# Performance work log

Hardware: AMD Instinct MI355X
Metric: run time of the kernel (lower is better)

## Reference

```python
import jax, jax.numpy as jnp
import numpy as np
import itertools

GRID_NUM = 12
VOXEL_SIZE = 0.12
OFFSET = GRID_NUM * VOXEL_SIZE / 2.0  # 0.72
G3 = GRID_NUM ** 3


def setup_inputs() -> dict:
    key = jax.random.key(0)
    k0, k1, k2, k3 = jax.random.split(key, 4)
    B, L0, L1, C = 4, 2048, 1024, 64
    x0 = jax.random.normal(k0, (B, L0, C), dtype=jnp.float32)
    x1 = jax.random.normal(k1, (B, L1, C), dtype=jnp.float32)
    # positions in [-0.3, 0.3) so delta_pos + OFFSET lies inside the grid [0, 1.44)
    pos0 = (jax.random.uniform(k2, (B, L0, 3), dtype=jnp.float32) - 0.5) * 0.6
    pos1 = (jax.random.uniform(k3, (B, L1, 3), dtype=jnp.float32) - 0.5) * 0.6
    return {"x0": x0, "x1": x1, "pos0": pos0, "pos1": pos1}


def _p2g_trilinear(pos, prob, seg, num_seg):
    """Trilinear point-to-grid splat.
    pos: (N,3) continuous coords in grid units' metric space; prob: (N,); seg: (N,) int segment id.
    Returns (num_seg, G3)."""
    c = pos / VOXEL_SIZE - 0.5          # voxel-center coordinates
    base = jnp.floor(c)
    frac = c - base                      # (N,3) in [0,1)
    base = base.astype(jnp.int32)
    out = jnp.zeros((num_seg * G3,), dtype=prob.dtype)
    for corner in itertools.product((0, 1), repeat=3):
        idx = base + jnp.asarray(corner, dtype=jnp.int32)  # (N,3)
        w = prob
        for d in range(3):
            w = w * (frac[:, d] if corner[d] else (1.0 - frac[:, d]))
        valid = jnp.all((idx >= 0) & (idx < GRID_NUM), axis=-1)
        flat = seg * G3 + idx[:, 0] * (GRID_NUM * GRID_NUM) + idx[:, 1] * GRID_NUM + idx[:, 2]
        flat = jnp.where(valid, flat, 0)
        out = out.at[flat].add(jnp.where(valid, w, 0.0))
    return out.reshape(num_seg, G3)


def reference(x0, x1, pos0, pos1):
    B, L0, C = x0.shape
    L1 = x1.shape[1]
    # scaled correlation + row softmax (stable; max-subtraction is math-identical)
    corr = jnp.einsum('blc,bmc->blm', x0, x1) / jnp.sqrt(jnp.asarray(C, x0.dtype))
    prob = jax.nn.softmax(corr, axis=-1)                       # (B,L0,L1)
    correspondence = jnp.einsum('blm,bmc->blc', prob, pos1)    # (B,L0,3)
    flow = correspondence - pos0
    # point-to-grid distribution of match probability over relative offsets
    delta = pos1[:, None, :, :] - pos0[:, :, None, :]          # (B,L0,L1,3)
    pos_f = delta.reshape(-1, 3) + OFFSET
    prob_f = prob.reshape(-1)
    N = B * L0 * L1
    seg = jnp.arange(N, dtype=jnp.int32) // L1                 # (N,) query-point segment id
    grid = _p2g_trilinear(pos_f, prob_f, seg, B * L0)          # (B*L0, G3)
    probs_grid = grid.reshape(B, L0, G3)
    return (flow, probs_grid)
```

## Files before the change

kernel.cpp:

```cpp
#include <hip/hip_runtime.h>
#include <stdint.h>

#define GRID_NUM 12
#define G3 1728
#define L0V 2048
#define L1V 1024
#define CV 64
#define RT 16
#define ERS 1032

typedef __attribute__((ext_vector_type(8))) short short8;
typedef __attribute__((ext_vector_type(4))) short short4v;
typedef __attribute__((ext_vector_type(4))) float f32x4;

__device__ __forceinline__ unsigned short f2bf(float f) {
    union { float f; unsigned u; } v; v.f = f;
    unsigned u = v.u;
    u += 0x7fffu + ((u >> 16) & 1u);
    return (unsigned short)(u >> 16);
}
__device__ __forceinline__ float bf2f(unsigned short h) {
    union { unsigned u; float f; } v; v.u = ((unsigned)h) << 16;
    return v.f;
}

__global__ __launch_bounds__(256) void corr_probs_kernel(
    const float* __restrict__ x0, const float* __restrict__ x1,
    const float* __restrict__ pos0, const float* __restrict__ pos1,
    float* __restrict__ out_flow, unsigned short* __restrict__ probs_bf,
    float* __restrict__ rscale)
{
    const int r0 = blockIdx.x * RT;
    const int b  = r0 >> 11;
    const int t  = threadIdx.x;
    const int lane = t & 63;
    const int w    = t >> 6;
    const int l15  = lane & 15;
    const int q    = lane >> 4;

    __shared__ __align__(16) short sX0h[RT * 64], sX0l[RT * 64];
    __shared__ __align__(16) short sX1h[64 * 64], sX1l[64 * 64];
    __shared__ __align__(16) float sp1[64 * 3];
    __shared__ __align__(16) short sE[RT * ERS];
    __shared__ float sred[4][RT][4];

    {
        const int row = t >> 4;
        const float4 v = ((const float4*)(x0 + (size_t)(r0 + row) * CV))[t & 15];
        const unsigned short h0 = f2bf(v.x), h1 = f2bf(v.y), h2 = f2bf(v.z), h3 = f2bf(v.w);
        const short4v hi = { (short)h0, (short)h1, (short)h2, (short)h3 };
        const short4v lo = { (short)f2bf(v.x - bf2f(h0)), (short)f2bf(v.y - bf2f(h1)),
                             (short)f2bf(v.z - bf2f(h2)), (short)f2bf(v.w - bf2f(h3)) };
        const int off = row * 128 + (((t & 15) * 8) ^ ((row & 7) << 4));
        *(short4v*)((char*)sX0h + off) = hi;
        *(short4v*)((char*)sX0l + off) = lo;
    }

    const float* x1b = x1 + (size_t)b * L1V * CV;
    const float* p1b = pos1 + (size_t)b * L1V * 3;

    float s_a = 0.f, cx_a = 0.f, cy_a = 0.f, cz_a = 0.f;

    for (int ch = 0; ch < L1V / 64; ++ch) {
        {
            const int key  = t >> 2;
            const int part = t & 3;
            const float4* src = (const float4*)(x1b + (size_t)(ch * 64 + key) * CV) + part * 4;
            const int sw = (key & 7) << 4;
            #pragma unroll
            for (int j = 0; j < 4; ++j) {
                const float4 v = src[j];
                const unsigned short h0 = f2bf(v.x), h1 = f2bf(v.y), h2 = f2bf(v.z), h3 = f2bf(v.w);
                const short4v hi = { (short)h0, (short)h1, (short)h2, (short)h3 };
                const short4v lo = { (short)f2bf(v.x - bf2f(h0)), (short)f2bf(v.y - bf2f(h1)),
                                     (short)f2bf(v.z - bf2f(h2)), (short)f2bf(v.w - bf2f(h3)) };
                const int off = key * 128 + (((part * 32) + j * 8) ^ sw);
                *(short4v*)((char*)sX1h + off) = hi;
                *(short4v*)((char*)sX1l + off) = lo;
            }
        }
        if (t < 192) sp1[t] = p1b[ch * 192 + t];
        __syncthreads();

        f32x4 acc = {0.f, 0.f, 0.f, 0.f};
        {
            const int ma    = w * 16 + l15;
            const int abase = ma * 128;
            const int asw   = (ma & 7) << 4;
            const int bbase = l15 * 128;
            const int bsw   = (l15 & 7) << 4;
            #pragma unroll
            for (int kk = 0; kk < 2; ++kk) {
                const int ka = (kk * 32 + q * 8) * 2;
                const short8 ah = *(const short8*)((const char*)sX1h + abase + (ka ^ asw));
                const short8 al = *(const short8*)((const char*)sX1l + abase + (ka ^ asw));
                const short8 bh = *(const short8*)((const char*)sX0h + bbase + (ka ^ bsw));
                const short8 bl = *(const short8*)((const char*)sX0l + bbase + (ka ^ bsw));
                acc = __builtin_amdgcn_mfma_f32_16x16x32_bf16(ah, bh, acc, 0, 0, 0);
                acc = __builtin_amdgcn_mfma_f32_16x16x32_bf16(ah, bl, acc, 0, 0, 0);
                acc = __builtin_amdgcn_mfma_f32_16x16x32_bf16(al, bh, acc, 0, 0, 0);
            }
        }
        unsigned short eb[4];
        #pragma unroll
        for (int rg = 0; rg < 4; ++rg) {
            const int kc = w * 16 + q * 4 + rg;
            const float e = __expf(acc[rg] * 0.125f);
            eb[rg] = f2bf(e);
            s_a += e;
            cx_a = fmaf(e, sp1[kc * 3 + 0], cx_a);
            cy_a = fmaf(e, sp1[kc * 3 + 1], cy_a);
            cz_a = fmaf(e, sp1[kc * 3 + 2], cz_a);
        }
        const short4v ev = { (short)eb[0], (short)eb[1], (short)eb[2], (short)eb[3] };
        *(short4v*)((char*)sE + l15 * (ERS * 2) + (ch * 64 + w * 16 + q * 4) * 2) = ev;
        __syncthreads();
    }

    s_a  += __shfl_xor(s_a, 16, 64);  s_a  += __shfl_xor(s_a, 32, 64);
    cx_a += __shfl_xor(cx_a, 16, 64); cx_a += __shfl_xor(cx_a, 32, 64);
    cy_a += __shfl_xor(cy_a, 16, 64); cy_a += __shfl_xor(cy_a, 32, 64);
    cz_a += __shfl_xor(cz_a, 16, 64); cz_a += __shfl_xor(cz_a, 32, 64);
    if (lane < 16) {
        sred[w][l15][0] = s_a;  sred[w][l15][1] = cx_a;
        sred[w][l15][2] = cy_a; sred[w][l15][3] = cz_a;
    }
    __syncthreads();

    if (t < RT) {
        const float S  = (sred[0][t][0] + sred[1][t][0]) + (sred[2][t][0] + sred[3][t][0]);
        const float CX = (sred[0][t][1] + sred[1][t][1]) + (sred[2][t][1] + sred[3][t][1]);
        const float CY = (sred[0][t][2] + sred[1][t][2]) + (sred[2][t][2] + sred[3][t][2]);
        const float CZ = (sred[0][t][3] + sred[1][t][3]) + (sred[2][t][3] + sred[3][t][3]);
        const float rs = 1.0f / S;
        rscale[r0 + t] = rs;
        out_flow[(r0 + t) * 3 + 0] = CX * rs - pos0[(r0 + t) * 3 + 0];
        out_flow[(r0 + t) * 3 + 1] = CY * rs - pos0[(r0 + t) * 3 + 1];
        out_flow[(r0 + t) * 3 + 2] = CZ * rs - pos0[(r0 + t) * 3 + 2];
    }

    #pragma unroll
    for (int i = 0; i < (RT * 128) / 256; ++i) {
        const int idx = i * 256 + t;
        const int row = idx >> 7;
        const int seg = idx & 127;
        const short8 v = *(const short8*)((const char*)sE + row * (ERS * 2) + seg * 16);
        *(short8*)(probs_bf + (size_t)(r0 + row) * L1V + seg * 8) = v;
    }
}

__global__ __launch_bounds__(256, 4) void splat_mfma_kernel(
    const unsigned short* __restrict__ probs_bf, const float* __restrict__ rscale,
    const float* __restrict__ pos0, const float* __restrict__ pos1,
    float* __restrict__ out_grid)
{
    const int t    = threadIdx.x;
    const int lane = t & 63;
    const int w    = t >> 6;
    const int r    = blockIdx.x * 4 + w;
    const int b    = r >> 11;

    __shared__ __align__(16) short sAll[4][4608];
    char* sR = (char*)sAll[w];
    char* sZ = (char*)sAll[w] + 8192;

    const float inv = 1.0f / 0.12f;
    const float p0x = pos0[r * 3 + 0];
    const float p0y = pos0[r * 3 + 1];
    const float p0z = pos0[r * 3 + 2];
    const float* p1b = pos1 + (size_t)b * L1V * 3;
    const unsigned short* prow = probs_bf + (size_t)r * L1V;

    const int mnx = (int)floorf((-0.3f - p0x + 0.72f) * inv - 0.5f);
    const int mny = (int)floorf((-0.3f - p0y + 0.72f) * inv - 0.5f);
    const int mnz = (int)floorf((-0.3f - p0z + 0.72f) * inv - 0.5f);

    {
        const short8 z8 = {0, 0, 0, 0, 0, 0, 0, 0};
        #pragma unroll
        for (int j = 0; j < 9; ++j)
            *(short8*)(sR + lane * 16 + j * 1024) = z8;
    }

    const int l15  = lane & 15;
    const int q16  = (lane >> 4) * 16;
    const int asw  = (l15 & 7) << 4;
    const int aoff0 = l15 * 128 + ((0  + q16) ^ asw);
    const int aoff1 = l15 * 128 + ((64 + q16) ^ asw);
    const int zrow = l15 & 7;
    const int bsw  = zrow << 4;
    const int boff0 = zrow * 128 + ((0  + q16) ^ bsw);
    const int boff1 = zrow * 128 + ((64 + q16) ^ bsw);
    const int lane2 = lane * 2;

    f32x4 acc[4];
    #pragma unroll
    for (int mt = 0; mt < 4; ++mt) acc[mt] = (f32x4){0.f, 0.f, 0.f, 0.f};

    char *P0 = sR + lane2, *P1 = sR + lane2, *P2 = sR + lane2,
         *P3 = sR + lane2, *P4 = sZ + lane2, *P5 = sZ + lane2;

    float px = p1b[lane * 3 + 0];
    float py = p1b[lane * 3 + 1];
    float pz = p1b[lane * 3 + 2];
    float pv = bf2f(prow[lane]);

    asm volatile("s_waitcnt lgkmcnt(0)" ::: "memory");

    for (int ch = 0; ch < 16; ++ch) {
        float nx = px, ny = py, nz = pz, nv = pv;
        if (ch < 15) {
            const int nk = (ch + 1) * 64 + lane;
            nx = p1b[nk * 3 + 0];
            ny = p1b[nk * 3 + 1];
            nz = p1b[nk * 3 + 2];
            nv = bf2f(prow[nk]);
        }

        const float ax = ((px - p0x) + 0.72f) * inv - 0.5f;
        const float ay = ((py - p0y) + 0.72f) * inv - 0.5f;
        const float az = ((pz - p0z) + 0.72f) * inv - 0.5f;
        const float fxf = floorf(ax), fyf = floorf(ay), fzf = floorf(az);
        const float fx = ax - fxf, fy = ay - fyf, fz = az - fzf;
        const int rix = (int)fxf - mnx;
        const int riy = (int)fyf - mny;
        const int riz = (int)fzf - mnz;
        const float wx0 = 1.f - fx, wy0 = 1.f - fy, wz0 = 1.f - fz;
        const float a0p = pv * wx0, a1p = pv * fx;
        const unsigned short r00 = f2bf(a0p * wy0), r01 = f2bf(a0p * fy);
        const unsigned short r10 = f2bf(a1p * wy0), r11 = f2bf(a1p * fy);
        const unsigned short z0 = f2bf(wz0), z1 = f2bf(fz);

        const int c00 = rix * 8 + riy;
        char* A0 = sR + (c00    ) * 128 + (lane2 ^ (((c00    ) & 7) << 4));
        char* A1 = sR + (c00 + 1) * 128 + (lane2 ^ (((c00 + 1) & 7) << 4));
        char* A2 = sR + (c00 + 8) * 128 + (lane2 ^ (((c00 + 8) & 7) << 4));
        char* A3 = sR + (c00 + 9) * 128 + (lane2 ^ (((c00 + 9) & 7) << 4));
        char* Z0a = sZ + riz * 128 + (lane2 ^ (riz << 4));
        char* Z1a = sZ + (riz + 1) * 128 + (lane2 ^ ((riz + 1) << 4));

        *(short*)P0 = 0; *(short*)P1 = 0; *(short*)P2 = 0;
        *(short*)P3 = 0; *(short*)P4 = 0; *(short*)P5 = 0;
        *(short*)A0 = (short)r00; *(short*)A1 = (short)r01;
        *(short*)A2 = (short)r10; *(short*)A3 = (short)r11;
        *(short*)Z0a = (short)z0; *(short*)Z1a = (short)z1;

        asm volatile("s_waitcnt lgkmcnt(0)" ::: "memory");
        __builtin_amdgcn_sched_barrier(0);

        const short8 b0 = *(const short8*)(sZ + boff0);
        const short8 b1 = *(const short8*)(sZ + boff1);
        #pragma unroll
        for (int mt = 0; mt < 4; ++mt) {
            const short8 a0 = *(const short8*)(sR + mt * 2048 + aoff0);
            const short8 a1 = *(const short8*)(sR + mt * 2048 + aoff1);
            acc[mt] = __builtin_amdgcn_mfma_f32_16x16x32_bf16(a0, b0, acc[mt], 0, 0, 0);
            acc[mt] = __builtin_amdgcn_mfma_f32_16x16x32_bf16(a1, b1, acc[mt], 0, 0, 0);
        }

        P0 = A0; P1 = A1; P2 = A2; P3 = A3; P4 = Z0a; P5 = Z1a;
        px = nx; py = ny; pz = nz; pv = nv;
    }

    const float rs = rscale[r];
    float* og = out_grid + (size_t)r * G3;
    {
        const float4 z4 = {0.f, 0.f, 0.f, 0.f};
        float4* og4 = (float4*)og;
        #pragma unroll
        for (int j = 0; j < 6; ++j) og4[j * 64 + lane] = z4;
        if (lane < 48) og4[384 + lane] = z4;
    }
    asm volatile("s_waitcnt vmcnt(0)" ::: "memory");

    const int zB = lane & 15;
    if (zB < 8) {
        const int gz = mnz + zB;
        if (gz <= 11) {
            const int h4 = (lane >> 4) * 4;
            const int rxm = 11 - mnx;
            const int rym = 11 - mny;
            float* base2 = og + mnx * 144 + mny * 12 + gz;
            #pragma unroll
            for (int mt = 0; mt < 4; ++mt) {
                #pragma unroll
                for (int rg = 0; rg < 4; ++rg) {
                    const int c  = mt * 16 + h4 + rg;
                    const int rx = c >> 3;
                    const int ry = c & 7;
                    if (rx <= rxm && ry <= rym)
                        base2[rx * 144 + ry * 12] = acc[mt][rg] * rs;
                }
            }
        }
    }
}

extern "C" void kernel_launch(void* const* d_in, const int* in_sizes, int n_in,
                              void* d_out, int out_size, void* d_ws, size_t ws_size,
                              hipStream_t stream) {
    const float* x0   = (const float*)d_in[0];
    const float* x1   = (const float*)d_in[1];
    const float* pos0 = (const float*)d_in[2];
    const float* pos1 = (const float*)d_in[3];
    float* out = (float*)d_out;

    const int B    = in_sizes[0] / (L0V * CV);
    const int rows = B * L0V;

    float* out_flow = out;
    float* out_grid = out + (size_t)rows * 3;

    unsigned short* probs_bf = (unsigned short*)d_ws;
    float* rscale = (float*)((char*)d_ws + (size_t)rows * L1V * sizeof(unsigned short));

    corr_probs_kernel<<<rows / RT, 256, 0, stream>>>(
        x0, x1, pos0, pos1, out_flow, probs_bf, rscale);
    splat_mfma_kernel<<<rows / 4, 256, 0, stream>>>(
        probs_bf, rscale, pos0, pos1, out_grid);
}
```

Before: 65.21 us.

## Pre-convert x1 to swizzled bf16 image and stream it via async LDS double buffer

Adds a small kernel that converts x1 once into a pre-swizzled hi/lo bf16 image, so corr_probs no longer redoes the fp32-to-split-bf16 conversion for every 16-row block. The main kernel now double-buffers 16KB chunks with global_load_lds and vmcnt waits instead of synchronous loads, preloads all of pos1 into LDS, and writes probs directly to global rather than staging them in LDS. It also drops an explicit lgkmcnt wait and sched_barrier in the splat kernel. The tradeoffs are an extra launch, a workspace buffer, and less coalesced probs stores. Removing the LDS wait before the MFMA reads in the splat kernel could be a correctness risk if the compiler does not insert it itself.

New measurement: 59.33 us. 1.1x faster.

```diff
diff --git a/kernel.cpp b/kernel.cpp
--- a/kernel.cpp
+++ b/kernel.cpp
@@ -7,7 +7,6 @@
 #define L1V 1024
 #define CV 64
 #define RT 16
-#define ERS 1032
 
 typedef __attribute__((ext_vector_type(8))) short short8;
 typedef __attribute__((ext_vector_type(4))) short short4v;
@@ -24,8 +23,42 @@
     return v.f;
 }
 
+__device__ __forceinline__ void gload16(const void* g, void* l) {
+    __builtin_amdgcn_global_load_lds(
+        (const __attribute__((address_space(1))) unsigned int*)(uintptr_t)g,
+        (__attribute__((address_space(3))) unsigned int*)(uintptr_t)l,
+        16, 0, 0);
+}
+
+__global__ __launch_bounds__(256) void cvt_x1_kernel(
+    const float* __restrict__ x1, unsigned short* __restrict__ ximg)
+{
+    const int g  = blockIdx.x * 256 + threadIdx.x;
+    const int kg = g >> 3;
+    const int j8 = g & 7;
+    const int key = kg & 1023;
+    const int ch  = key >> 6;
+    const int kk  = key & 63;
+    const int bi  = kg >> 10;
+
+    const float4* src = (const float4*)(x1 + (size_t)kg * CV + j8 * 8);
+    const float4 v0 = src[0], v1 = src[1];
+    const float vv[8] = {v0.x, v0.y, v0.z, v0.w, v1.x, v1.y, v1.z, v1.w};
+    short8 hi, lo;
+    #pragma unroll
+    for (int i = 0; i < 8; ++i) {
+        const unsigned short h = f2bf(vv[i]);
+        hi[i] = (short)h;
+        lo[i] = (short)f2bf(vv[i] - bf2f(h));
+    }
+    char* base = (char*)ximg + ((size_t)(bi * 16 + ch)) * 16384;
+    const int off = kk * 128 + ((j8 * 16) ^ ((kk & 7) << 4));
+    *(short8*)(base + off) = hi;
+    *(short8*)(base + 8192 + off) = lo;
+}
+
 __global__ __launch_bounds__(256) void corr_probs_kernel(
-    const float* __restrict__ x0, const float* __restrict__ x1,
+    const float* __restrict__ x0, const unsigned short* __restrict__ ximg,
     const float* __restrict__ pos0, const float* __restrict__ pos1,
     float* __restrict__ out_flow, unsigned short* __restrict__ probs_bf,
     float* __restrict__ rscale)
@@ -39,9 +72,8 @@
     const int q    = lane >> 4;
 
     __shared__ __align__(16) short sX0h[RT * 64], sX0l[RT * 64];
-    __shared__ __align__(16) short sX1h[64 * 64], sX1l[64 * 64];
-    __shared__ __align__(16) float sp1[64 * 3];
-    __shared__ __align__(16) short sE[RT * ERS];
+    __shared__ __align__(16) char  sX1[2][16384];
+    __shared__ __align__(16) float sp1[L1V * 3];
     __shared__ float sred[4][RT][4];
 
     {
@@ -55,56 +87,61 @@
         *(short4v*)((char*)sX0h + off) = hi;
         *(short4v*)((char*)sX0l + off) = lo;
     }
-
-    const float* x1b = x1 + (size_t)b * L1V * CV;
-    const float* p1b = pos1 + (size_t)b * L1V * 3;
+    {
+        const float4* ps = (const float4*)(pos1 + (size_t)b * L1V * 3);
+        #pragma unroll
+        for (int i = 0; i < 3; ++i)
+            ((float4*)sp1)[i * 256 + t] = ps[i * 256 + t];
+    }
+
+    const char* img = (const char*)ximg + (size_t)b * (16 * 16384);
+    #pragma unroll
+    for (int i = 0; i < 4; ++i)
+        gload16(img + (w * 4 + i) * 1024 + lane * 16,
+                sX1[0] + (w * 4 + i) * 1024);
+    __syncthreads();
+
+    const int ma    = w * 16 + l15;
+    const int abase = ma * 128;
+    const int asw   = (ma & 7) << 4;
+    const int bbase = l15 * 128;
+    const int bsw   = (l15 & 7) << 4;
 
     float s_a = 0.f, cx_a = 0.f, cy_a = 0.f, cz_a = 0.f;
 
-    for (int ch = 0; ch < L1V / 64; ++ch) {
-        {
-            const int key  = t >> 2;
-            const int part = t & 3;
-            const float4* src = (const float4*)(x1b + (size_t)(ch * 64 + key) * CV) + part * 4;
-            const int sw = (key & 7) << 4;
+    for (int ch = 0; ch < 16; ++ch) {
+        const int buf = ch & 1;
+        if (ch < 15) {
+            const char* s = img + (ch + 1) * 16384;
+            char* d = sX1[buf ^ 1];
             #pragma unroll
-            for (int j = 0; j < 4; ++j) {
-                const float4 v = src[j];
-                const unsigned short h0 = f2bf(v.x), h1 = f2bf(v.y), h2 = f2bf(v.z), h3 = f2bf(v.w);
-                const short4v hi = { (short)h0, (short)h1, (short)h2, (short)h3 };
-                const short4v lo = { (short)f2bf(v.x - bf2f(h0)), (short)f2bf(v.y - bf2f(h1)),
-                                     (short)f2bf(v.z - bf2f(h2)), (short)f2bf(v.w - bf2f(h3)) };
-                const int off = key * 128 + (((part * 32) + j * 8) ^ sw);
-                *(short4v*)((char*)sX1h + off) = hi;
-                *(short4v*)((char*)sX1l + off) = lo;
-            }
-        }
-        if (t < 192) sp1[t] = p1b[ch * 192 + t];
-        __syncthreads();
-
+            for (int i = 0; i < 4; ++i)
+                gload16(s + (w * 4 + i) * 1024 + lane * 16, d + (w * 4 + i) * 1024);
+            asm volatile("s_waitcnt vmcnt(4)" ::: "memory");
+        } else {
+            asm volatile("s_waitcnt vmcnt(1)" ::: "memory");
+        }
+        __builtin_amdgcn_s_barrier();
+
+        const char* Xh = sX1[buf];
+        const char* Xl = Xh + 8192;
         f32x4 acc = {0.f, 0.f, 0.f, 0.f};
-        {
-            const int ma    = w * 16 + l15;
-            const int abase = ma * 128;
-            const int asw   = (ma & 7) << 4;
-            const int bbase = l15 * 128;
-            const int bsw   = (l15 & 7) << 4;
-            #pragma unroll
-            for (int kk = 0; kk < 2; ++kk) {
-                const int ka = (kk * 32 + q * 8) * 2;
-                const short8 ah = *(const short8*)((const char*)sX1h + abase + (ka ^ asw));
-                const short8 al = *(const short8*)((const char*)sX1l + abase + (ka ^ asw));
-                const short8 bh = *(const short8*)((const char*)sX0h + bbase + (ka ^ bsw));
-                const short8 bl = *(const short8*)((const char*)sX0l + bbase + (ka ^ bsw));
-                acc = __builtin_amdgcn_mfma_f32_16x16x32_bf16(ah, bh, acc, 0, 0, 0);
-                acc = __builtin_amdgcn_mfma_f32_16x16x32_bf16(ah, bl, acc, 0, 0, 0);
-                acc = __builtin_amdgcn_mfma_f32_16x16x32_bf16(al, bh, acc, 0, 0, 0);
-            }
-        }
+        #pragma unroll
+        for (int kk = 0; kk < 2; ++kk) {
+            const int ka = (kk * 32 + q * 8) * 2;
+            const short8 ah = *(const short8*)(Xh + abase + (ka ^ asw));
+            const short8 al = *(const short8*)(Xl + abase + (ka ^ asw));
+            const short8 bh = *(const short8*)((const char*)sX0h + bbase + (ka ^ bsw));
+            const short8 bl = *(const short8*)((const char*)sX0l + bbase + (ka ^ bsw));
+            acc = __builtin_amdgcn_mfma_f32_16x16x32_bf16(ah, bh, acc, 0, 0, 0);
+            acc = __builtin_amdgcn_mfma_f32_16x16x32_bf16(ah, bl, acc, 0, 0, 0);
+            acc = __builtin_amdgcn_mfma_f32_16x16x32_bf16(al, bh, acc, 0, 0, 0);
+        }
+
         unsigned short eb[4];
         #pragma unroll
         for (int rg = 0; rg < 4; ++rg) {
-            const int kc = w * 16 + q * 4 + rg;
+            const int kc = ch * 64 + w * 16 + q * 4 + rg;
             const float e = __expf(acc[rg] * 0.125f);
             eb[rg] = f2bf(e);
             s_a += e;
@@ -113,8 +150,9 @@
             cz_a = fmaf(e, sp1[kc * 3 + 2], cz_a);
         }
         const short4v ev = { (short)eb[0], (short)eb[1], (short)eb[2], (short)eb[3] };
-        *(short4v*)((char*)sE + l15 * (ERS * 2) + (ch * 64 + w * 16 + q * 4) * 2) = ev;
-        __syncthreads();
+        *(short4v*)(probs_bf + (size_t)(r0 + l15) * L1V + ch * 64 + w * 16 + q * 4) = ev;
+
+        __builtin_amdgcn_s_barrier();
     }
 
     s_a  += __shfl_xor(s_a, 16, 64);  s_a  += __shfl_xor(s_a, 32, 64);
@@ -137,15 +175,6 @@
         out_flow[(r0 + t) * 3 + 0] = CX * rs - pos0[(r0 + t) * 3 + 0];
         out_flow[(r0 + t) * 3 + 1] = CY * rs - pos0[(r0 + t) * 3 + 1];
         out_flow[(r0 + t) * 3 + 2] = CZ * rs - pos0[(r0 + t) * 3 + 2];
-    }
-
-    #pragma unroll
-    for (int i = 0; i < (RT * 128) / 256; ++i) {
-        const int idx = i * 256 + t;
-        const int row = idx >> 7;
-        const int seg = idx & 127;
-        const short8 v = *(const short8*)((const char*)sE + row * (ERS * 2) + seg * 16);
-        *(short8*)(probs_bf + (size_t)(r0 + row) * L1V + seg * 8) = v;
     }
 }
 
@@ -244,9 +273,6 @@
         *(short*)A0 = (short)r00; *(short*)A1 = (short)r01;
         *(short*)A2 = (short)r10; *(short*)A3 = (short)r11;
         *(short*)Z0a = (short)z0; *(short*)Z1a = (short)z1;
-
-        asm volatile("s_waitcnt lgkmcnt(0)" ::: "memory");
-        __builtin_amdgcn_sched_barrier(0);
 
         const short8 b0 = *(const short8*)(sZ + boff0);
         const short8 b1 = *(const short8*)(sZ + boff1);
@@ -313,9 +339,11 @@
 
     unsigned short* probs_bf = (unsigned short*)d_ws;
     float* rscale = (float*)((char*)d_ws + (size_t)rows * L1V * sizeof(unsigned short));
-
+    unsigned short* ximg = (unsigned short*)((char*)rscale + (size_t)rows * sizeof(float));
+
+    cvt_x1_kernel<<<(B * L1V * CV / 8) / 256, 256, 0, stream>>>(x1, ximg);
     corr_probs_kernel<<<rows / RT, 256, 0, stream>>>(
-        x0, x1, pos0, pos1, out_flow, probs_bf, rscale);
+        x0, ximg, pos0, pos1, out_flow, probs_bf, rscale);
     splat_mfma_kernel<<<rows / 4, 256, 0, stream>>>(
         probs_bf, rscale, pos0, pos1, out_grid);
 }
```
